# Performance work log

Measured on AMD Instinct MI355X. Metric: run time of the kernel, lower is better.

Reference implementation:

```python
import jax, jax.numpy as jnp
import numpy as np

B, S, D = 2, 4096, 256
H, DH, DM = 8, 32, 1024
ROPE_BASE = 10000.0
LN_EPS = 1e-5


def _layer_norm(x, g, b):
    mu = jnp.mean(x, axis=-1, keepdims=True)
    var = jnp.mean(jnp.square(x - mu), axis=-1, keepdims=True)
    return (x - mu) * jax.lax.rsqrt(var + LN_EPS) * g + b


def _rope(x):
    # x: [b, s, h, d_head]; lucidrains interleaved-pair RoPE
    s, d = x.shape[1], x.shape[-1]
    inv_freq = 1.0 / (ROPE_BASE ** (jnp.arange(0, d, 2, dtype=jnp.float32) / d))  # [d/2]
    freqs = jnp.arange(s, dtype=jnp.float32)[:, None] * inv_freq[None, :]          # [s, d/2]
    freqs = jnp.repeat(freqs, 2, axis=-1)                                          # [s, d]
    cos = jnp.cos(freqs)[None, :, None, :]
    sin = jnp.sin(freqs)[None, :, None, :]
    x1, x2 = x[..., 0::2], x[..., 1::2]
    rot = jnp.stack((-x2, x1), axis=-1).reshape(x.shape)
    return x * cos + rot * sin


def setup_inputs() -> dict:
    key = jax.random.key(0)
    ks = jax.random.split(key, 8)
    sw = 1.0 / np.sqrt(D)
    return {
        "x": jax.random.normal(ks[0], (B, S, D), jnp.float32),
        "Wq": jax.random.normal(ks[1], (D, D), jnp.float32) * sw,
        "Wk": jax.random.normal(ks[2], (D, D), jnp.float32) * sw,
        "Wv": jax.random.normal(ks[3], (D, D), jnp.float32) * sw,
        "Wo": jax.random.normal(ks[4], (D, D), jnp.float32) * sw,
        "ln1_g": jnp.ones((D,), jnp.float32),
        "ln1_b": jnp.zeros((D,), jnp.float32),
        "ln2_g": jnp.ones((D,), jnp.float32),
        "ln2_b": jnp.zeros((D,), jnp.float32),
        "W2": jax.random.normal(ks[5], (DM, D), jnp.float32) * sw,
        "b2": jnp.zeros((DM,), jnp.float32),
        "W3": jax.random.normal(ks[6], (D, DM), jnp.float32) * (1.0 / np.sqrt(DM)),
        "b3": jnp.zeros((D,), jnp.float32),
    }


def reference(x, Wq, Wk, Wv, Wo, ln1_g, ln1_b, ln2_g, ln2_b, W2, b2, W3, b3):
    b, s, d = x.shape
    h, dh = H, DH
    xn = _layer_norm(x, ln1_g, ln1_b)
    q = (xn @ Wq.T).reshape(b, s, h, dh)
    k = (xn @ Wk.T).reshape(b, s, h, dh)
    v = (xn @ Wv.T).reshape(b, s, h, dh)
    q = _rope(q)
    k = _rope(k)
    # scores: [b, h, q, k] (full matrix, matching original implementation)
    scores = jnp.einsum('bqhd,bkhd->bhqk', q, k) / np.sqrt(dh)
    attn = jax.nn.softmax(scores, axis=-1)
    out = jnp.einsum('bhqk,bkhd->bqhd', attn, v).reshape(b, s, d)
    out = out @ Wo.T
    mlp_in = out + x
    y = _layer_norm(mlp_in, ln2_g, ln2_b)
    y = jax.nn.gelu(y @ W2.T + b2, approximate=False)
    y = y @ W3.T + b3
    return y + mlp_in
```

## Files before the change

kernel.cpp:

```cpp
#include <hip/hip_runtime.h>
#include <math.h>

#define D 256
#define S 4096
#define H 8
#define DH 32
#define DM 1024
#define NTOK 8192

typedef __attribute__((ext_vector_type(8))) short short8;
typedef __attribute__((ext_vector_type(4))) float f32x4;

#define QSCALE (0.17677669529663687f * 1.4426950408889634f)

__device__ inline unsigned short f2bf(float f) {
    union { float f; unsigned u; } v; v.f = f;
    unsigned r = v.u + 0x7fffu + ((v.u >> 16) & 1u);
    return (unsigned short)(r >> 16);
}
__device__ inline void gload16(const void* g, void* l) {
    __builtin_amdgcn_global_load_lds((const __attribute__((address_space(1))) void*)g,
                                     (__attribute__((address_space(3))) void*)l, 16, 0, 0);
}

__device__ inline short8 pack_p(f32x4 s0, f32x4 s1) {
    unsigned u0[4], u1[4];
    #pragma unroll
    for (int i = 0; i < 4; ++i) {
        union { float f; unsigned u; } c0, c1;
        c0.f = __builtin_amdgcn_exp2f(s0[i]);
        c1.f = __builtin_amdgcn_exp2f(s1[i]);
        u0[i] = c0.u;
        u1[i] = c1.u;
    }
    union { unsigned u[4]; short8 s; } pk;
    pk.u[0] = __builtin_amdgcn_perm(u0[1], u0[0], 0x07060302u);
    pk.u[1] = __builtin_amdgcn_perm(u0[3], u0[2], 0x07060302u);
    pk.u[2] = __builtin_amdgcn_perm(u1[1], u1[0], 0x07060302u);
    pk.u[3] = __builtin_amdgcn_perm(u1[3], u1[2], 0x07060302u);
    return pk.s;
}

__global__ void prep(const float* __restrict__ Wq, const float* __restrict__ Wk,
                     const float* __restrict__ Wv, const float* __restrict__ Wo,
                     const float* __restrict__ W2, const float* __restrict__ W3,
                     unsigned short* __restrict__ wqkv, unsigned short* __restrict__ wo_b,
                     unsigned short* __restrict__ w2_b, unsigned short* __restrict__ w3_b,
                     float* __restrict__ ct, float* __restrict__ st,
                     const float* __restrict__ x, const float* __restrict__ g,
                     const float* __restrict__ b, unsigned short* __restrict__ xn) {
    int blk = blockIdx.x;
    if (blk < 3328) {
        int i = blk * 256 + threadIdx.x;
        if (i < 196608) {
            const float* s = (i < 65536) ? Wq : ((i < 131072) ? Wk : Wv);
            wqkv[i] = f2bf(s[i & 65535]);
        } else if (i < 262144) {
            wo_b[i - 196608] = f2bf(Wo[i - 196608]);
        } else if (i < 524288) {
            w2_b[i - 262144] = f2bf(W2[i - 262144]);
        } else if (i < 786432) {
            w3_b[i - 524288] = f2bf(W3[i - 524288]);
        } else {
            int j = i - 786432;
            int spos = j >> 4, pi = j & 15;
            float inv_freq = powf(10000.0f, -(float)(2 * pi) / 32.0f);
            float fr = (float)spos * inv_freq;
            ct[j] = cosf(fr);
            st[j] = sinf(fr);
        }
        return;
    }
    int l = threadIdx.x & 63;
    int row = (blk - 3328) * 4 + (threadIdx.x >> 6);
    const float4 v = *(const float4*)(x + (size_t)row * D + l * 4);
    float s  = v.x + v.y + v.z + v.w;
    float s2 = v.x * v.x + v.y * v.y + v.z * v.z + v.w * v.w;
    #pragma unroll
    for (int off = 32; off > 0; off >>= 1) {
        s  += __shfl_xor(s, off, 64);
        s2 += __shfl_xor(s2, off, 64);
    }
    float mu  = s * (1.0f / D);
    float var = s2 * (1.0f / D) - mu * mu;
    float rs  = rsqrtf(var + 1e-5f);
    const float4 gg = *(const float4*)(g + l * 4);
    const float4 bb = *(const float4*)(b + l * 4);
    ushort4 o;
    o.x = f2bf((v.x - mu) * rs * gg.x + bb.x);
    o.y = f2bf((v.y - mu) * rs * gg.y + bb.y);
    o.z = f2bf((v.z - mu) * rs * gg.z + bb.z);
    o.w = f2bf((v.w - mu) * rs * gg.w + bb.w);
    *(ushort4*)(xn + (size_t)row * D + l * 4) = o;
}

__global__ void ln_kernel(const float* __restrict__ x, const float* __restrict__ g,
                          const float* __restrict__ b, unsigned short* __restrict__ out) {
    int l = threadIdx.x & 63;
    int row = blockIdx.x * 4 + (threadIdx.x >> 6);
    const float4 v = *(const float4*)(x + (size_t)row * D + l * 4);
    float s  = v.x + v.y + v.z + v.w;
    float s2 = v.x * v.x + v.y * v.y + v.z * v.z + v.w * v.w;
    #pragma unroll
    for (int off = 32; off > 0; off >>= 1) {
        s  += __shfl_xor(s, off, 64);
        s2 += __shfl_xor(s2, off, 64);
    }
    float mu  = s * (1.0f / D);
    float var = s2 * (1.0f / D) - mu * mu;
    float rs  = rsqrtf(var + 1e-5f);
    const float4 gg = *(const float4*)(g + l * 4);
    const float4 bb = *(const float4*)(b + l * 4);
    ushort4 o;
    o.x = f2bf((v.x - mu) * rs * gg.x + bb.x);
    o.y = f2bf((v.y - mu) * rs * gg.y + bb.y);
    o.z = f2bf((v.z - mu) * rs * gg.z + bb.z);
    o.w = f2bf((v.w - mu) * rs * gg.w + bb.w);
    *(ushort4*)(out + (size_t)row * D + l * 4) = o;
}

__global__ __launch_bounds__(256) void gemm64b(const unsigned short* __restrict__ A,
        const unsigned short* __restrict__ Bw, void* __restrict__ outp,
        unsigned short* __restrict__ vt,
        const float* __restrict__ bias,
        const float* __restrict__ ct, const float* __restrict__ st,
        int N, int K, int mode) {
    __shared__ unsigned short As[2][64 * 64];
    __shared__ unsigned short Bs[2][64 * 64];
    int tid = threadIdx.x;
    int w = tid >> 6, l = tid & 63;
    int lm = l & 15, lg = l >> 4;
    int wm = (w >> 1) * 32, wn = (w & 1) * 32;
    int bm = blockIdx.x * 64, bn = blockIdx.y * 64;
    int r1 = tid >> 3, pc = tid & 7;
    int pcx = (pc ^ (r1 & 7)) * 8;
    const unsigned short* Ag1 = A + (size_t)(bm + r1) * K + pcx;
    const unsigned short* Ag2 = A + (size_t)(bm + 32 + r1) * K + pcx;
    const unsigned short* Bg1 = Bw + (size_t)(bn + r1) * K + pcx;
    const unsigned short* Bg2 = Bw + (size_t)(bn + 32 + r1) * K + pcx;
    const int swz = lm & 7;
    f32x4 acc[2][2] = {};

    gload16(Ag1, &As[0][w * 512]);
    gload16(Ag2, &As[0][2048 + w * 512]);
    gload16(Bg1, &Bs[0][w * 512]);
    gload16(Bg2, &Bs[0][2048 + w * 512]);
    for (int k0 = 0; k0 < K; k0 += 64) {
        int cur = (k0 >> 6) & 1;
        __syncthreads();
        if (k0 + 64 < K) {
            gload16(Ag1 + k0 + 64, &As[1 - cur][w * 512]);
            gload16(Ag2 + k0 + 64, &As[1 - cur][2048 + w * 512]);
            gload16(Bg1 + k0 + 64, &Bs[1 - cur][w * 512]);
            gload16(Bg2 + k0 + 64, &Bs[1 - cur][2048 + w * 512]);
        }
        #pragma unroll
        for (int j = 0; j < 2; ++j) {
            int ch = ((j * 4 + lg) ^ swz) * 8;
            short8 af[2], bf[2];
            #pragma unroll
            for (int i = 0; i < 2; ++i) af[i] = *(const short8*)&As[cur][(wm + i * 16 + lm) * 64 + ch];
            #pragma unroll
            for (int i = 0; i < 2; ++i) bf[i] = *(const short8*)&Bs[cur][(wn + i * 16 + lm) * 64 + ch];
            #pragma unroll
            for (int mi = 0; mi < 2; ++mi)
                #pragma unroll
                for (int ni = 0; ni < 2; ++ni)
                    acc[mi][ni] = __builtin_amdgcn_mfma_f32_16x16x32_bf16(af[mi], bf[ni], acc[mi][ni], 0, 0, 0);
        }
    }

    if (mode == 0) {
        if (bn >= 512) {
            #pragma unroll
            for (int mi = 0; mi < 2; ++mi) {
                #pragma unroll
                for (int ni = 0; ni < 2; ++ni) {
                    int ng = bn + wn + ni * 16 + lm - 512;
                    int hh = ng >> 5, dh = ng & 31;
                    int mg0 = bm + wm + mi * 16 + lg * 4;
                    int bb = mg0 >> 12, ss = mg0 & 4095;
                    ushort4 pv;
                    pv.x = f2bf(acc[mi][ni][0]); pv.y = f2bf(acc[mi][ni][1]);
                    pv.z = f2bf(acc[mi][ni][2]); pv.w = f2bf(acc[mi][ni][3]);
                    *(ushort4*)(vt + ((size_t)((bb * 8 + hh) * 32 + dh)) * S + ss) = pv;
                }
            }
        } else {
            #pragma unroll
            for (int mi = 0; mi < 2; ++mi) {
                #pragma unroll
                for (int ni = 0; ni < 2; ++ni) {
                    int ng = bn + wn + ni * 16 + lm;
                    int pi = (ng & 31) >> 1;
                    float sgn = (ng & 1) ? 1.f : -1.f;
                    float qs  = (ng < 256) ? QSCALE : 1.f;
                    #pragma unroll
                    for (int r2 = 0; r2 < 4; ++r2) {
                        int mg = bm + wm + mi * 16 + lg * 4 + r2;
                        int spos = mg & (S - 1);
                        float vv = acc[mi][ni][r2];
                        float pv = __shfl_xor(vv, 1, 64);
                        float cs = ct[spos * 16 + pi];
                        float sn = st[spos * 16 + pi];
                        float ov = (vv * cs + sgn * pv * sn) * qs;
                        ((unsigned short*)outp)[(size_t)mg * N + ng] = f2bf(ov);
                    }
                }
            }
        }
        return;
    }
    #pragma unroll
    for (int mi = 0; mi < 2; ++mi) {
        #pragma unroll
        for (int ni = 0; ni < 2; ++ni) {
            int ng = bn + wn + ni * 16 + lm;
            #pragma unroll
            for (int r2 = 0; r2 < 4; ++r2) {
                int mg = bm + wm + mi * 16 + lg * 4 + r2;
                float t = acc[mi][ni][r2] + bias[ng];
                ((unsigned short*)outp)[(size_t)mg * N + ng] =
                    f2bf(0.5f * t * (1.0f + erff(t * 0.70710678118654752f)));
            }
        }
    }
}

__global__ __launch_bounds__(256) void gemm32(const unsigned short* __restrict__ A,
        const unsigned short* __restrict__ Bw, void* __restrict__ outp,
        const float* __restrict__ bias, const float* __restrict__ res,
        int N, int K, int mode) {
    __shared__ unsigned short As[2][64 * 128];
    __shared__ unsigned short Bs[2][64 * 128];
    int tid = threadIdx.x;
    int w = tid >> 6, l = tid & 63;
    int lm = l & 15, lg = l >> 4;
    int wm = (w >> 1) * 32, wn = (w & 1) * 32;
    int bm = blockIdx.x * 64, bn = blockIdx.y * 64;
    int r1 = tid >> 4, pc = tid & 15;
    int pcx = (pc ^ (r1 & 7)) * 8;
    const unsigned short* Ag1 = A + (size_t)(bm + r1) * K + pcx;
    const unsigned short* Ag2 = A + (size_t)(bm + 16 + r1) * K + pcx;
    const unsigned short* Ag3 = A + (size_t)(bm + 32 + r1) * K + pcx;
    const unsigned short* Ag4 = A + (size_t)(bm + 48 + r1) * K + pcx;
    const unsigned short* Bg1 = Bw + (size_t)(bn + r1) * K + pcx;
    const unsigned short* Bg2 = Bw + (size_t)(bn + 16 + r1) * K + pcx;
    const unsigned short* Bg3 = Bw + (size_t)(bn + 32 + r1) * K + pcx;
    const unsigned short* Bg4 = Bw + (size_t)(bn + 48 + r1) * K + pcx;
    const int swz = lm & 7;
    f32x4 acc[2][2] = {};

    gload16(Ag1, &As[0][w * 512]);
    gload16(Ag2, &As[0][2048 + w * 512]);
    gload16(Ag3, &As[0][4096 + w * 512]);
    gload16(Ag4, &As[0][6144 + w * 512]);
    gload16(Bg1, &Bs[0][w * 512]);
    gload16(Bg2, &Bs[0][2048 + w * 512]);
    gload16(Bg3, &Bs[0][4096 + w * 512]);
    gload16(Bg4, &Bs[0][6144 + w * 512]);
    for (int k0 = 0; k0 < K; k0 += 128) {
        int cur = (k0 >> 7) & 1;
        __syncthreads();
        if (k0 + 128 < K) {
            gload16(Ag1 + k0 + 128, &As[1 - cur][w * 512]);
            gload16(Ag2 + k0 + 128, &As[1 - cur][2048 + w * 512]);
            gload16(Ag3 + k0 + 128, &As[1 - cur][4096 + w * 512]);
            gload16(Ag4 + k0 + 128, &As[1 - cur][6144 + w * 512]);
            gload16(Bg1 + k0 + 128, &Bs[1 - cur][w * 512]);
            gload16(Bg2 + k0 + 128, &Bs[1 - cur][2048 + w * 512]);
            gload16(Bg3 + k0 + 128, &Bs[1 - cur][4096 + w * 512]);
            gload16(Bg4 + k0 + 128, &Bs[1 - cur][6144 + w * 512]);
        }
        #pragma unroll
        for (int j = 0; j < 4; ++j) {
            int ch = ((j * 4 + lg) ^ swz) * 8;
            short8 af[2], bf[2];
            #pragma unroll
            for (int i = 0; i < 2; ++i) af[i] = *(const short8*)&As[cur][(wm + i * 16 + lm) * 128 + ch];
            #pragma unroll
            for (int i = 0; i < 2; ++i) bf[i] = *(const short8*)&Bs[cur][(wn + i * 16 + lm) * 128 + ch];
            #pragma unroll
            for (int mi = 0; mi < 2; ++mi)
                #pragma unroll
                for (int ni = 0; ni < 2; ++ni)
                    acc[mi][ni] = __builtin_amdgcn_mfma_f32_16x16x32_bf16(af[mi], bf[ni], acc[mi][ni], 0, 0, 0);
        }
    }

    #pragma unroll
    for (int mi = 0; mi < 2; ++mi) {
        #pragma unroll
        for (int ni = 0; ni < 2; ++ni) {
            int ng = bn + wn + ni * 16 + lm;
            #pragma unroll
            for (int r2 = 0; r2 < 4; ++r2) {
                int mg = bm + wm + mi * 16 + lg * 4 + r2;
                float v = acc[mi][ni][r2];
                size_t idx = (size_t)mg * N + ng;
                if (mode == 1) {
                    ((float*)outp)[idx] = v + res[idx];
                } else {
                    ((float*)outp)[idx] = v + bias[ng] + res[idx];
                }
            }
        }
    }
}

__global__ __launch_bounds__(512, 4) void attn_kernel(const unsigned short* __restrict__ Cq,
        const unsigned short* __restrict__ vt, unsigned short* __restrict__ out) {
    __shared__ unsigned short Ks[2][3][64][32];
    __shared__ unsigned short Vs[2][3][32][64];
    int tid = threadIdx.x;
    int w = tid >> 6, l = tid & 63;
    int grp = w >> 2, ws = w & 3;
    int lm = l & 15, lg = l >> 4;
    int qt = blockIdx.x >> 4;
    int bh = blockIdx.x & 15;
    int bb = bh >> 3, h = bh & 7;
    int q0 = qt * 128 + ws * 32;

    const short8 qfa = *(const short8*)(Cq + ((size_t)(bb * S + q0 + lm)) * 768 + h * DH + lg * 8);
    const short8 qfb = *(const short8*)(Cq + ((size_t)(bb * S + q0 + 16 + lm)) * 768 + h * DH + lg * 8);

    union { unsigned short us[8]; short8 s; } onesu;
    {
        unsigned short ov = (lm == 0) ? (unsigned short)0x3F80 : (unsigned short)0;
        #pragma unroll
        for (int i = 0; i < 8; ++i) onesu.us[i] = ov;
    }
    const short8 onef = onesu.s;

    int p = ws * 16 + (l >> 2);
    int krow = ((p >> 5) << 5) + (((p >> 2) & 3) << 3) + (((p >> 4) & 1) << 2) + (p & 3);
    const unsigned short* kg = Cq + ((size_t)(bb * S)) * 768 + 256 + h * 32
                               + (size_t)krow * 768 + ((l & 3) ^ ((l >> 3) & 3)) * 8;
    const unsigned short* vg = vt + ((size_t)(bh * 32 + ws * 8 + (l >> 3))) * S + ((l & 7) ^ (l >> 3)) * 8;
    const int kswz = (lm >> 1) & 3;
    const int vswz = lm & 7;

    f32x4 o0a = {0.f, 0.f, 0.f, 0.f}, o1a = {0.f, 0.f, 0.f, 0.f}, o2a = {0.f, 0.f, 0.f, 0.f};
    f32x4 o0b = {0.f, 0.f, 0.f, 0.f}, o1b = {0.f, 0.f, 0.f, 0.f}, o2b = {0.f, 0.f, 0.f, 0.f};
    const f32x4 z = {0.f, 0.f, 0.f, 0.f};

    gload16(kg + (size_t)grp * 64 * 768,       &Ks[grp][0][ws * 16][0]);
    gload16(vg + (size_t)grp * 64,             &Vs[grp][0][ws * 8][0]);
    gload16(kg + (size_t)(2 + grp) * 64 * 768, &Ks[grp][1][ws * 16][0]);
    gload16(vg + (size_t)(2 + grp) * 64,       &Vs[grp][1][ws * 8][0]);
    asm volatile("s_waitcnt vmcnt(4)" ::: "memory");

#define ATTN_STEP(J, CUR, NXT) do {                                                          \
    asm volatile("s_waitcnt vmcnt(2) lgkmcnt(0)" ::: "memory");                              \
    __builtin_amdgcn_s_barrier();                                                            \
    __builtin_amdgcn_sched_barrier(0);                                                       \
    int tt_ = (J) + 2; if (tt_ > 31) tt_ = 31;                                               \
    size_t tg_ = (size_t)(2 * tt_ + grp);                                                    \
    gload16(kg + tg_ * 64 * 768, &Ks[grp][NXT][ws * 16][0]);                                 \
    gload16(vg + tg_ * 64,       &Vs[grp][NXT][ws * 8][0]);                                  \
    _Pragma("unroll")                                                                        \
    for (int half = 0; half < 2; ++half) {                                                   \
        short8 kf0 = *(const short8*)&Ks[grp][CUR][half * 32 + lm][(lg ^ kswz) * 8];         \
        short8 kf1 = *(const short8*)&Ks[grp][CUR][half * 32 + 16 + lm][(lg ^ kswz) * 8];    \
        __builtin_amdgcn_s_setprio(1);                                                       \
        f32x4 s0a = __builtin_amdgcn_mfma_f32_16x16x32_bf16(kf0, qfa, z, 0, 0, 0);           \
        f32x4 s1a = __builtin_amdgcn_mfma_f32_16x16x32_bf16(kf1, qfa, z, 0, 0, 0);           \
        f32x4 s0b = __builtin_amdgcn_mfma_f32_16x16x32_bf16(kf0, qfb, z, 0, 0, 0);           \
        f32x4 s1b = __builtin_amdgcn_mfma_f32_16x16x32_bf16(kf1, qfb, z, 0, 0, 0);           \
        __builtin_amdgcn_s_setprio(0);                                                       \
        short8 pfa = pack_p(s0a, s1a);                                                       \
        short8 pfb = pack_p(s0b, s1b);                                                       \
        int vc = ((half * 4 + lg) ^ vswz) * 8;                                               \
        short8 va0 = *(const short8*)&Vs[grp][CUR][lm][vc];                                  \
        short8 va1 = *(const short8*)&Vs[grp][CUR][16 + lm][vc];                             \
        __builtin_amdgcn_s_setprio(1);                                                       \
        o0a = __builtin_amdgcn_mfma_f32_16x16x32_bf16(va0, pfa, o0a, 0, 0, 0);               \
        o1a = __builtin_amdgcn_mfma_f32_16x16x32_bf16(va1, pfa, o1a, 0, 0, 0);               \
        o2a = __builtin_amdgcn_mfma_f32_16x16x32_bf16(onef, pfa, o2a, 0, 0, 0);               \
        o0b = __builtin_amdgcn_mfma_f32_16x16x32_bf16(va0, pfb, o0b, 0, 0, 0);               \
        o1b = __builtin_amdgcn_mfma_f32_16x16x32_bf16(va1, pfb, o1b, 0, 0, 0);               \
        o2b = __builtin_amdgcn_mfma_f32_16x16x32_bf16(onef, pfb, o2b, 0, 0, 0);               \
        __builtin_amdgcn_s_setprio(0);                                                       \
    }                                                                                        \
} while (0)

    for (int j3 = 0; j3 < 30; j3 += 3) {
        ATTN_STEP(j3,     0, 2);
        ATTN_STEP(j3 + 1, 1, 0);
        ATTN_STEP(j3 + 2, 2, 1);
    }
    ATTN_STEP(30, 0, 2);
    ATTN_STEP(31, 1, 0);
#undef ATTN_STEP

    f32x4* Red = (f32x4*)&Ks[0][0][0][0];
    float* Den = (float*)&Vs[0][0][0][0];
    __syncthreads();
    if (grp) {
        Red[(0 * 4 + ws) * 64 + l] = o0a;
        Red[(1 * 4 + ws) * 64 + l] = o1a;
        Red[(2 * 4 + ws) * 64 + l] = o0b;
        Red[(3 * 4 + ws) * 64 + l] = o1b;
        Den[(ws * 2 + 0) * 64 + l] = o2a[0];
        Den[(ws * 2 + 1) * 64 + l] = o2b[0];
    }
    __syncthreads();
    if (!grp) {
        f32x4 a0 = Red[(0 * 4 + ws) * 64 + l];
        f32x4 a1 = Red[(1 * 4 + ws) * 64 + l];
        f32x4 a2 = Red[(2 * 4 + ws) * 64 + l];
        f32x4 a3 = Red[(3 * 4 + ws) * 64 + l];
        float dda = o2a[0] + Den[(ws * 2 + 0) * 64 + l];
        float ddb = o2b[0] + Den[(ws * 2 + 1) * 64 + l];
        #pragma unroll
        for (int i = 0; i < 4; ++i) {
            o0a[i] += a0[i]; o1a[i] += a1[i];
            o0b[i] += a2[i]; o1b[i] += a3[i];
        }
        float inva = 1.0f / __shfl(dda, lm, 64);
        float invb = 1.0f / __shfl(ddb, lm, 64);
        ushort4 r0, r1;
        r0.x = f2bf(o0a[0] * inva); r0.y = f2bf(o0a[1] * inva);
        r0.z = f2bf(o0a[2] * inva); r0.w = f2bf(o0a[3] * inva);
        r1.x = f2bf(o1a[0] * inva); r1.y = f2bf(o1a[1] * inva);
        r1.z = f2bf(o1a[2] * inva); r1.w = f2bf(o1a[3] * inva);
        unsigned short* ob = out + ((size_t)(bb * S + q0 + lm)) * D + h * DH;
        *(ushort4*)(ob + lg * 4)      = r0;
        *(ushort4*)(ob + 16 + lg * 4) = r1;
        r0.x = f2bf(o0b[0] * invb); r0.y = f2bf(o0b[1] * invb);
        r0.z = f2bf(o0b[2] * invb); r0.w = f2bf(o0b[3] * invb);
        r1.x = f2bf(o1b[0] * invb); r1.y = f2bf(o1b[1] * invb);
        r1.z = f2bf(o1b[2] * invb); r1.w = f2bf(o1b[3] * invb);
        unsigned short* ob2 = out + ((size_t)(bb * S + q0 + 16 + lm)) * D + h * DH;
        *(ushort4*)(ob2 + lg * 4)      = r0;
        *(ushort4*)(ob2 + 16 + lg * 4) = r1;
    }
}

extern "C" void kernel_launch(void* const* d_in, const int* in_sizes, int n_in,
                              void* d_out, int out_size, void* d_ws, size_t ws_size,
                              hipStream_t stream) {
    const float* x     = (const float*)d_in[0];
    const float* Wq    = (const float*)d_in[1];
    const float* Wk    = (const float*)d_in[2];
    const float* Wv    = (const float*)d_in[3];
    const float* Wo    = (const float*)d_in[4];
    const float* ln1_g = (const float*)d_in[5];
    const float* ln1_b = (const float*)d_in[6];
    const float* ln2_g = (const float*)d_in[7];
    const float* ln2_b = (const float*)d_in[8];
    const float* W2    = (const float*)d_in[9];
    const float* b2    = (const float*)d_in[10];
    const float* W3    = (const float*)d_in[11];
    const float* b3    = (const float*)d_in[12];

    char* w8 = (char*)d_ws;
    unsigned short* wqkv = (unsigned short*)(w8);
    unsigned short* wo_b = (unsigned short*)(w8 + 393216);
    unsigned short* w2_b = (unsigned short*)(w8 + 524288);
    unsigned short* w3_b = (unsigned short*)(w8 + 1048576);
    float*          ct   = (float*)(w8 + 1572864);
    float*          st   = (float*)(w8 + 1835008);
    unsigned short* xn   = (unsigned short*)(w8 + 2097152);
    unsigned short* Cq   = (unsigned short*)(w8 + 6291456);
    unsigned short* hb   = Cq;
    unsigned short* vtb  = (unsigned short*)(w8 + 23068672);
    unsigned short* ab   = (unsigned short*)(w8 + 27262976);
    float*          mlpin= (float*)(w8 + 31457280);
    unsigned short* yn   = xn;

    prep<<<5376, 256, 0, stream>>>(Wq, Wk, Wv, Wo, W2, W3, wqkv, wo_b, w2_b, w3_b,
                                   ct, st, x, ln1_g, ln1_b, xn);
    gemm64b<<<dim3(128, 12), 256, 0, stream>>>(xn, wqkv, Cq, vtb, nullptr, ct, st, 768, 256, 0);
    attn_kernel<<<512, 512, 0, stream>>>(Cq, vtb, ab);
    gemm32<<<dim3(128, 4), 256, 0, stream>>>(ab, wo_b, mlpin, nullptr, x, 256, 256, 1);
    ln_kernel<<<NTOK / 4, 256, 0, stream>>>(mlpin, ln2_g, ln2_b, yn);
    gemm64b<<<dim3(128, 16), 256, 0, stream>>>(yn, w2_b, hb, nullptr, b2, nullptr, nullptr, 1024, 256, 2);
    gemm32<<<dim3(128, 4), 256, 0, stream>>>(hb, w3_b, (float*)d_out, b3, mlpin, 256, 1024, 3);
}
```

Baseline: 181.0 us.

## Split attention keys across four wave groups with smaller query tiles

Each attention block now handles 64 queries instead of 128. The key/value sequence is split across four groups of two waves each, instead of two groups of four, using 32-key tiles. The grid doubles to 1024 blocks, the occupancy hint in launch bounds rises, and the LDS reduction sums partials from three groups instead of one. The goal is more parallelism and shorter per-block work, at the cost of loading each K/V tile for fewer queries and a larger final reduction.

```diff
diff --git a/kernel.cpp b/kernel.cpp
--- a/kernel.cpp
+++ b/kernel.cpp
@@ -179,11 +179,11 @@
                     int ng = bn + wn + ni * 16 + lm - 512;
                     int hh = ng >> 5, dh = ng & 31;
                     int mg0 = bm + wm + mi * 16 + lg * 4;
-                    int bb = mg0 >> 12, ss = mg0 & 4095;
+                    int bbx = mg0 >> 12, ss = mg0 & 4095;
                     ushort4 pv;
                     pv.x = f2bf(acc[mi][ni][0]); pv.y = f2bf(acc[mi][ni][1]);
                     pv.z = f2bf(acc[mi][ni][2]); pv.w = f2bf(acc[mi][ni][3]);
-                    *(ushort4*)(vt + ((size_t)((bb * 8 + hh) * 32 + dh)) * S + ss) = pv;
+                    *(ushort4*)(vt + ((size_t)((bbx * 8 + hh) * 32 + dh)) * S + ss) = pv;
                 }
             }
         } else {
@@ -308,18 +308,18 @@
     }
 }
 
-__global__ __launch_bounds__(512, 4) void attn_kernel(const unsigned short* __restrict__ Cq,
+__global__ __launch_bounds__(512, 6) void attn_kernel(const unsigned short* __restrict__ Cq,
         const unsigned short* __restrict__ vt, unsigned short* __restrict__ out) {
-    __shared__ unsigned short Ks[2][3][64][32];
-    __shared__ unsigned short Vs[2][3][32][64];
+    __shared__ unsigned short Ks[4][3][32][32];
+    __shared__ unsigned short Vs[4][3][32][32];
     int tid = threadIdx.x;
     int w = tid >> 6, l = tid & 63;
-    int grp = w >> 2, ws = w & 3;
+    int grp = w >> 1, ws = w & 1;
     int lm = l & 15, lg = l >> 4;
     int qt = blockIdx.x >> 4;
     int bh = blockIdx.x & 15;
     int bb = bh >> 3, h = bh & 7;
-    int q0 = qt * 128 + ws * 32;
+    int q0 = qt * 64 + ws * 32;
 
     const short8 qfa = *(const short8*)(Cq + ((size_t)(bb * S + q0 + lm)) * 768 + h * DH + lg * 8);
     const short8 qfb = *(const short8*)(Cq + ((size_t)(bb * S + q0 + 16 + lm)) * 768 + h * DH + lg * 8);
@@ -333,21 +333,22 @@
     const short8 onef = onesu.s;
 
     int p = ws * 16 + (l >> 2);
-    int krow = ((p >> 5) << 5) + (((p >> 2) & 3) << 3) + (((p >> 4) & 1) << 2) + (p & 3);
+    int krow = (((p >> 2) & 3) << 3) + (((p >> 4) & 1) << 2) + (p & 3);
     const unsigned short* kg = Cq + ((size_t)(bb * S)) * 768 + 256 + h * 32
                                + (size_t)krow * 768 + ((l & 3) ^ ((l >> 3) & 3)) * 8;
-    const unsigned short* vg = vt + ((size_t)(bh * 32 + ws * 8 + (l >> 3))) * S + ((l & 7) ^ (l >> 3)) * 8;
+    const unsigned short* vg = vt + ((size_t)(bh * 32 + ws * 16 + (l >> 2))) * S
+                               + ((l & 3) ^ ((l >> 4) & 3)) * 8;
     const int kswz = (lm >> 1) & 3;
-    const int vswz = lm & 7;
+    const int vswz = (lm >> 2) & 3;
 
     f32x4 o0a = {0.f, 0.f, 0.f, 0.f}, o1a = {0.f, 0.f, 0.f, 0.f}, o2a = {0.f, 0.f, 0.f, 0.f};
     f32x4 o0b = {0.f, 0.f, 0.f, 0.f}, o1b = {0.f, 0.f, 0.f, 0.f}, o2b = {0.f, 0.f, 0.f, 0.f};
     const f32x4 z = {0.f, 0.f, 0.f, 0.f};
 
-    gload16(kg + (size_t)grp * 64 * 768,       &Ks[grp][0][ws * 16][0]);
-    gload16(vg + (size_t)grp * 64,             &Vs[grp][0][ws * 8][0]);
-    gload16(kg + (size_t)(2 + grp) * 64 * 768, &Ks[grp][1][ws * 16][0]);
-    gload16(vg + (size_t)(2 + grp) * 64,       &Vs[grp][1][ws * 8][0]);
+    gload16(kg + (size_t)grp * 32 * 768,       &Ks[grp][0][ws * 16][0]);
+    gload16(vg + (size_t)grp * 32,             &Vs[grp][0][ws * 16][0]);
+    gload16(kg + (size_t)(4 + grp) * 32 * 768, &Ks[grp][1][ws * 16][0]);
+    gload16(vg + (size_t)(4 + grp) * 32,       &Vs[grp][1][ws * 16][0]);
     asm volatile("s_waitcnt vmcnt(4)" ::: "memory");
 
 #define ATTN_STEP(J, CUR, NXT) do {                                                          \
@@ -355,33 +356,30 @@
     __builtin_amdgcn_s_barrier();                                                            \
     __builtin_amdgcn_sched_barrier(0);                                                       \
     int tt_ = (J) + 2; if (tt_ > 31) tt_ = 31;                                               \
-    size_t tg_ = (size_t)(2 * tt_ + grp);                                                    \
-    gload16(kg + tg_ * 64 * 768, &Ks[grp][NXT][ws * 16][0]);                                 \
-    gload16(vg + tg_ * 64,       &Vs[grp][NXT][ws * 8][0]);                                  \
-    _Pragma("unroll")                                                                        \
-    for (int half = 0; half < 2; ++half) {                                                   \
-        short8 kf0 = *(const short8*)&Ks[grp][CUR][half * 32 + lm][(lg ^ kswz) * 8];         \
-        short8 kf1 = *(const short8*)&Ks[grp][CUR][half * 32 + 16 + lm][(lg ^ kswz) * 8];    \
-        __builtin_amdgcn_s_setprio(1);                                                       \
-        f32x4 s0a = __builtin_amdgcn_mfma_f32_16x16x32_bf16(kf0, qfa, z, 0, 0, 0);           \
-        f32x4 s1a = __builtin_amdgcn_mfma_f32_16x16x32_bf16(kf1, qfa, z, 0, 0, 0);           \
-        f32x4 s0b = __builtin_amdgcn_mfma_f32_16x16x32_bf16(kf0, qfb, z, 0, 0, 0);           \
-        f32x4 s1b = __builtin_amdgcn_mfma_f32_16x16x32_bf16(kf1, qfb, z, 0, 0, 0);           \
-        __builtin_amdgcn_s_setprio(0);                                                       \
-        short8 pfa = pack_p(s0a, s1a);                                                       \
-        short8 pfb = pack_p(s0b, s1b);                                                       \
-        int vc = ((half * 4 + lg) ^ vswz) * 8;                                               \
-        short8 va0 = *(const short8*)&Vs[grp][CUR][lm][vc];                                  \
-        short8 va1 = *(const short8*)&Vs[grp][CUR][16 + lm][vc];                             \
-        __builtin_amdgcn_s_setprio(1);                                                       \
-        o0a = __builtin_amdgcn_mfma_f32_16x16x32_bf16(va0, pfa, o0a, 0, 0, 0);               \
-        o1a = __builtin_amdgcn_mfma_f32_16x16x32_bf16(va1, pfa, o1a, 0, 0, 0);               \
-        o2a = __builtin_amdgcn_mfma_f32_16x16x32_bf16(onef, pfa, o2a, 0, 0, 0);               \
-        o0b = __builtin_amdgcn_mfma_f32_16x16x32_bf16(va0, pfb, o0b, 0, 0, 0);               \
-        o1b = __builtin_amdgcn_mfma_f32_16x16x32_bf16(va1, pfb, o1b, 0, 0, 0);               \
-        o2b = __builtin_amdgcn_mfma_f32_16x16x32_bf16(onef, pfb, o2b, 0, 0, 0);               \
-        __builtin_amdgcn_s_setprio(0);                                                       \
-    }                                                                                        \
+    size_t tg_ = (size_t)(4 * tt_ + grp);                                                    \
+    gload16(kg + tg_ * 32 * 768, &Ks[grp][NXT][ws * 16][0]);                                 \
+    gload16(vg + tg_ * 32,       &Vs[grp][NXT][ws * 16][0]);                                 \
+    short8 kf0 = *(const short8*)&Ks[grp][CUR][lm][(lg ^ kswz) * 8];                         \
+    short8 kf1 = *(const short8*)&Ks[grp][CUR][16 + lm][(lg ^ kswz) * 8];                    \
+    __builtin_amdgcn_s_setprio(1);                                                           \
+    f32x4 s0a = __builtin_amdgcn_mfma_f32_16x16x32_bf16(kf0, qfa, z, 0, 0, 0);               \
+    f32x4 s1a = __builtin_amdgcn_mfma_f32_16x16x32_bf16(kf1, qfa, z, 0, 0, 0);               \
+    f32x4 s0b = __builtin_amdgcn_mfma_f32_16x16x32_bf16(kf0, qfb, z, 0, 0, 0);               \
+    f32x4 s1b = __builtin_amdgcn_mfma_f32_16x16x32_bf16(kf1, qfb, z, 0, 0, 0);               \
+    __builtin_amdgcn_s_setprio(0);                                                           \
+    short8 pfa = pack_p(s0a, s1a);                                                           \
+    short8 pfb = pack_p(s0b, s1b);                                                           \
+    int vc = (lg ^ vswz) * 8;                                                                \
+    short8 va0 = *(const short8*)&Vs[grp][CUR][lm][vc];                                      \
+    short8 va1 = *(const short8*)&Vs[grp][CUR][16 + lm][vc];                                 \
+    __builtin_amdgcn_s_setprio(1);                                                           \
+    o0a = __builtin_amdgcn_mfma_f32_16x16x32_bf16(va0, pfa, o0a, 0, 0, 0);                   \
+    o1a = __builtin_amdgcn_mfma_f32_16x16x32_bf16(va1, pfa, o1a, 0, 0, 0);                   \
+    o2a = __builtin_amdgcn_mfma_f32_16x16x32_bf16(onef, pfa, o2a, 0, 0, 0);                  \
+    o0b = __builtin_amdgcn_mfma_f32_16x16x32_bf16(va0, pfb, o0b, 0, 0, 0);                   \
+    o1b = __builtin_amdgcn_mfma_f32_16x16x32_bf16(va1, pfb, o1b, 0, 0, 0);                   \
+    o2b = __builtin_amdgcn_mfma_f32_16x16x32_bf16(onef, pfb, o2b, 0, 0, 0);                  \
+    __builtin_amdgcn_s_setprio(0);                                                           \
 } while (0)
 
     for (int j3 = 0; j3 < 30; j3 += 3) {
@@ -397,25 +395,31 @@
     float* Den = (float*)&Vs[0][0][0][0];
     __syncthreads();
     if (grp) {
-        Red[(0 * 4 + ws) * 64 + l] = o0a;
-        Red[(1 * 4 + ws) * 64 + l] = o1a;
-        Red[(2 * 4 + ws) * 64 + l] = o0b;
-        Red[(3 * 4 + ws) * 64 + l] = o1b;
-        Den[(ws * 2 + 0) * 64 + l] = o2a[0];
-        Den[(ws * 2 + 1) * 64 + l] = o2b[0];
+        int gi = (grp - 1) * 2 + ws;
+        Red[(gi * 4 + 0) * 64 + l] = o0a;
+        Red[(gi * 4 + 1) * 64 + l] = o1a;
+        Red[(gi * 4 + 2) * 64 + l] = o0b;
+        Red[(gi * 4 + 3) * 64 + l] = o1b;
+        Den[(gi * 2 + 0) * 64 + l] = o2a[0];
+        Den[(gi * 2 + 1) * 64 + l] = o2b[0];
     }
     __syncthreads();
     if (!grp) {
-        f32x4 a0 = Red[(0 * 4 + ws) * 64 + l];
-        f32x4 a1 = Red[(1 * 4 + ws) * 64 + l];
-        f32x4 a2 = Red[(2 * 4 + ws) * 64 + l];
-        f32x4 a3 = Red[(3 * 4 + ws) * 64 + l];
-        float dda = o2a[0] + Den[(ws * 2 + 0) * 64 + l];
-        float ddb = o2b[0] + Den[(ws * 2 + 1) * 64 + l];
-        #pragma unroll
-        for (int i = 0; i < 4; ++i) {
-            o0a[i] += a0[i]; o1a[i] += a1[i];
-            o0b[i] += a2[i]; o1b[i] += a3[i];
+        float dda = o2a[0], ddb = o2b[0];
+        #pragma unroll
+        for (int g = 0; g < 3; ++g) {
+            int gi = g * 2 + ws;
+            f32x4 a0 = Red[(gi * 4 + 0) * 64 + l];
+            f32x4 a1 = Red[(gi * 4 + 1) * 64 + l];
+            f32x4 a2 = Red[(gi * 4 + 2) * 64 + l];
+            f32x4 a3 = Red[(gi * 4 + 3) * 64 + l];
+            #pragma unroll
+            for (int i = 0; i < 4; ++i) {
+                o0a[i] += a0[i]; o1a[i] += a1[i];
+                o0b[i] += a2[i]; o1b[i] += a3[i];
+            }
+            dda += Den[(gi * 2 + 0) * 64 + l];
+            ddb += Den[(gi * 2 + 1) * 64 + l];
         }
         float inva = 1.0f / __shfl(dda, lm, 64);
         float invb = 1.0f / __shfl(ddb, lm, 64);
@@ -472,7 +476,7 @@
     prep<<<5376, 256, 0, stream>>>(Wq, Wk, Wv, Wo, W2, W3, wqkv, wo_b, w2_b, w3_b,
                                    ct, st, x, ln1_g, ln1_b, xn);
     gemm64b<<<dim3(128, 12), 256, 0, stream>>>(xn, wqkv, Cq, vtb, nullptr, ct, st, 768, 256, 0);
-    attn_kernel<<<512, 512, 0, stream>>>(Cq, vtb, ab);
+    attn_kernel<<<1024, 512, 0, stream>>>(Cq, vtb, ab);
     gemm32<<<dim3(128, 4), 256, 0, stream>>>(ab, wo_b, mlpin, nullptr, x, 256, 256, 1);
     ln_kernel<<<NTOK / 4, 256, 0, stream>>>(mlpin, ln2_g, ln2_b, yn);
     gemm64b<<<dim3(128, 16), 256, 0, stream>>>(yn, w2_b, hb, nullptr, b2, nullptr, nullptr, 1024, 256, 2);
```

Result: slower. 186.3 us (+3.0%).
